# Kernel optimization log

Measured on AMD Instinct MI355X. Metric: run time of the kernel, lower is better.

The kernel has to match this reference:

```python
import jax, jax.numpy as jnp
import numpy as np

NUM_CLASSES = 512
WIDTH = 2  # triangular half-width in bins
MODE = 'triangular'
SIGMA = 1.0
B = 65536


def setup_inputs() -> dict:
    key = jax.random.key(0)
    k1, k2 = jax.random.split(key)
    logits = jax.random.normal(k1, (B, NUM_CLASSES), dtype=jnp.float32)
    targets = jax.random.randint(k2, (B,), 0, NUM_CLASSES, dtype=jnp.int64)
    return {"logits": logits, "targets": targets}


def _soft_targets(targets, C, dtype):
    # Vectorized replacement of the per-row Python loop.
    c = targets[:, None]                     # [B, 1]
    j = jnp.arange(C)[None, :]               # [1, C]
    d = jnp.abs(j - c)                       # [B, C] bin distance
    if MODE == 'triangular':
        w = jnp.where(d <= WIDTH, (WIDTH + 1 - d).astype(dtype), jnp.zeros((), dtype))
    elif MODE == 'log-triangular':
        w = jnp.where(d <= WIDTH, jnp.exp(-d.astype(dtype)), jnp.zeros((), dtype))
    else:  # gaussian
        w = jnp.where(d <= WIDTH,
                      jnp.exp(-0.5 * (d.astype(dtype) / SIGMA) ** 2),
                      jnp.zeros((), dtype))
    return w / jnp.sum(w, axis=1, keepdims=True)


def reference(logits, targets):
    Bsz, C = logits.shape
    st = _soft_targets(targets, C, logits.dtype)        # [B, C] normalized soft labels
    logp = jax.nn.log_softmax(logits, axis=1)            # [B, C]
    # KL(st || softmax(logits)) with 0*log0 = 0, matching F.kl_div(log_probs, st)
    safe_st = jnp.where(st > 0, st, jnp.ones((), logits.dtype))
    kl = jnp.where(st > 0, st * (jnp.log(safe_st) - logp), jnp.zeros((), logits.dtype))
    return jnp.sum(kl) / Bsz  # batchmean
```

## Files before the change

kernel.cpp:

```cpp
#include <hip/hip_runtime.h>

#define CDIM 512
#define BROWS 65536
#define NBLK 4096

typedef float floatx4 __attribute__((ext_vector_type(4)));

__device__ __forceinline__ float wpart(int j, int t, float x) {
    int d = j - t;
    int ad = d < 0 ? -d : d;
    return (ad <= 2) ? (float)(3 - ad) * x : 0.0f;
}

__global__ __launch_bounds__(256) void SoftTargetLoss_62646392979666_kernel(
        const float* __restrict__ logits,
        const int* __restrict__ targets,
        float* __restrict__ partials) {
    const int lane = threadIdx.x & 63;
    const int wid  = threadIdx.x >> 6;
    const int row0 = (blockIdx.x * 4 + wid) * 4;

    floatx4 a[4], b[4];
    int t[4];
    #pragma unroll
    for (int r = 0; r < 4; ++r) {
        const floatx4* rp = (const floatx4*)(logits + (size_t)(row0 + r) * CDIM);
        a[r] = __builtin_nontemporal_load(rp + lane);
        b[r] = __builtin_nontemporal_load(rp + lane + 64);
    }
    #pragma unroll
    for (int r = 0; r < 4; ++r) t[r] = targets[row0 + r];

    float acc = 0.0f;
    float s[4];
    #pragma unroll
    for (int r = 0; r < 4; ++r) {
        s[r] = __expf(a[r].x) + __expf(a[r].y) + __expf(a[r].z) + __expf(a[r].w)
             + __expf(b[r].x) + __expf(b[r].y) + __expf(b[r].z) + __expf(b[r].w);

        const int j0 = lane * 4, j1 = 256 + lane * 4;
        const int tt = t[r];
        float dp = wpart(j0,     tt, a[r].x) + wpart(j0 + 1, tt, a[r].y)
                 + wpart(j0 + 2, tt, a[r].z) + wpart(j0 + 3, tt, a[r].w)
                 + wpart(j1,     tt, b[r].x) + wpart(j1 + 1, tt, b[r].y)
                 + wpart(j1 + 2, tt, b[r].z) + wpart(j1 + 3, tt, b[r].w);

        float H, invW;
        if (tt >= 2 && tt <= CDIM - 3) { H = -1.52295508f; invW = 1.0f / 9.0f; }
        else if (tt == 0 || tt == CDIM - 1) { H = -1.01140427f; invW = 1.0f / 6.0f; }
        else { H = -1.32088835f; invW = 1.0f / 8.0f; }

        acc = fmaf(dp, -invW, acc);
        acc += H * (1.0f / 64.0f);
    }

    #pragma unroll
    for (int off = 32; off >= 1; off >>= 1) {
        #pragma unroll
        for (int r = 0; r < 4; ++r) s[r] += __shfl_xor(s[r], off, 64);
    }
    #pragma unroll
    for (int r = 0; r < 4; ++r) acc += __logf(s[r]) * (1.0f / 64.0f);

    #pragma unroll
    for (int off = 32; off >= 1; off >>= 1) acc += __shfl_xor(acc, off, 64);

    __shared__ float sred[4];
    if (lane == 0) sred[wid] = acc;
    __syncthreads();
    if (threadIdx.x == 0)
        partials[blockIdx.x] = sred[0] + sred[1] + sred[2] + sred[3];
}

__global__ __launch_bounds__(256) void stl_reduce(
        const float* __restrict__ partials, float* __restrict__ out) {
    float v = 0.0f;
    for (int i = threadIdx.x; i < NBLK; i += 256) v += partials[i];
    #pragma unroll
    for (int off = 32; off >= 1; off >>= 1) v += __shfl_xor(v, off, 64);
    __shared__ float sred[4];
    if ((threadIdx.x & 63) == 0) sred[threadIdx.x >> 6] = v;
    __syncthreads();
    if (threadIdx.x == 0)
        out[0] = (sred[0] + sred[1] + sred[2] + sred[3]) * (1.0f / (float)BROWS);
}

extern "C" void kernel_launch(void* const* d_in, const int* in_sizes, int n_in,
                              void* d_out, int out_size, void* d_ws, size_t ws_size,
                              hipStream_t stream) {
    const float* logits   = (const float*)d_in[0];
    const int*   targets  = (const int*)d_in[1];
    float*       out      = (float*)d_out;
    float*       partials = (float*)d_ws;

    SoftTargetLoss_62646392979666_kernel<<<NBLK, 256, 0, stream>>>(logits, targets, partials);
    stl_reduce<<<1, 256, 0, stream>>>(partials, out);
}
```

Before: 183.1 us.

## Process 16 rows per wave with double-buffered register prefetch

Each wave now handles 16 rows in four iterations instead of 4 rows. The loads for the next group of 4 rows are issued before computing the current group, using two register buffers, and the grid shrinks to 1024 blocks with a launch-bounds occupancy hint. This is meant to overlap memory latency with the exp and shuffle work and to cut block launch overhead and partials traffic, at the cost of higher register pressure and fewer waves for latency hiding. The final reduce loop is also unrolled over the smaller partials array.

Measured after the change: 217.2 us. 1.19x slower.

```diff
diff --git a/kernel.cpp b/kernel.cpp
--- a/kernel.cpp
+++ b/kernel.cpp
@@ -2,7 +2,8 @@
 
 #define CDIM 512
 #define BROWS 65536
-#define NBLK 4096
+#define NBLK 1024
+#define ITERS 4
 
 typedef float floatx4 __attribute__((ext_vector_type(4)));
 
@@ -12,55 +13,73 @@
     return (ad <= 2) ? (float)(3 - ad) * x : 0.0f;
 }
 
-__global__ __launch_bounds__(256) void SoftTargetLoss_62646392979666_kernel(
+__global__ __launch_bounds__(256, 4) void SoftTargetLoss_62646392979666_kernel(
         const float* __restrict__ logits,
         const int* __restrict__ targets,
         float* __restrict__ partials) {
     const int lane = threadIdx.x & 63;
     const int wid  = threadIdx.x >> 6;
-    const int row0 = (blockIdx.x * 4 + wid) * 4;
+    const int gw   = blockIdx.x * 4 + wid;
+    const size_t row0 = (size_t)gw * (ITERS * 4);
+    const floatx4* rp = (const floatx4*)logits + row0 * (CDIM / 4);
 
-    floatx4 a[4], b[4];
-    int t[4];
+    int t[ITERS * 4];
+    #pragma unroll
+    for (int r = 0; r < ITERS * 4; ++r) t[r] = targets[row0 + r];
+
+    floatx4 A[2][4], B[2][4];
     #pragma unroll
     for (int r = 0; r < 4; ++r) {
-        const floatx4* rp = (const floatx4*)(logits + (size_t)(row0 + r) * CDIM);
-        a[r] = __builtin_nontemporal_load(rp + lane);
-        b[r] = __builtin_nontemporal_load(rp + lane + 64);
+        A[0][r] = __builtin_nontemporal_load(rp + (size_t)r * (CDIM / 4) + lane);
+        B[0][r] = __builtin_nontemporal_load(rp + (size_t)r * (CDIM / 4) + 64 + lane);
     }
-    #pragma unroll
-    for (int r = 0; r < 4; ++r) t[r] = targets[row0 + r];
 
     float acc = 0.0f;
-    float s[4];
-    #pragma unroll
-    for (int r = 0; r < 4; ++r) {
-        s[r] = __expf(a[r].x) + __expf(a[r].y) + __expf(a[r].z) + __expf(a[r].w)
-             + __expf(b[r].x) + __expf(b[r].y) + __expf(b[r].z) + __expf(b[r].w);
-
-        const int j0 = lane * 4, j1 = 256 + lane * 4;
-        const int tt = t[r];
-        float dp = wpart(j0,     tt, a[r].x) + wpart(j0 + 1, tt, a[r].y)
-                 + wpart(j0 + 2, tt, a[r].z) + wpart(j0 + 3, tt, a[r].w)
-                 + wpart(j1,     tt, b[r].x) + wpart(j1 + 1, tt, b[r].y)
-                 + wpart(j1 + 2, tt, b[r].z) + wpart(j1 + 3, tt, b[r].w);
-
-        float H, invW;
-        if (tt >= 2 && tt <= CDIM - 3) { H = -1.52295508f; invW = 1.0f / 9.0f; }
-        else if (tt == 0 || tt == CDIM - 1) { H = -1.01140427f; invW = 1.0f / 6.0f; }
-        else { H = -1.32088835f; invW = 1.0f / 8.0f; }
-
-        acc = fmaf(dp, -invW, acc);
-        acc += H * (1.0f / 64.0f);
-    }
 
     #pragma unroll
-    for (int off = 32; off >= 1; off >>= 1) {
+    for (int it = 0; it < ITERS; ++it) {
+        const int cb = it & 1;
+        if (it + 1 < ITERS) {
+            const int nb = cb ^ 1;
+            #pragma unroll
+            for (int r = 0; r < 4; ++r) {
+                const size_t v = (size_t)(it + 1) * 4 * (CDIM / 4) + (size_t)r * (CDIM / 4);
+                A[nb][r] = __builtin_nontemporal_load(rp + v + lane);
+                B[nb][r] = __builtin_nontemporal_load(rp + v + 64 + lane);
+            }
+        }
+
+        float s[4];
         #pragma unroll
-        for (int r = 0; r < 4; ++r) s[r] += __shfl_xor(s[r], off, 64);
+        for (int r = 0; r < 4; ++r) {
+            const floatx4 a = A[cb][r], b = B[cb][r];
+            s[r] = __expf(a.x) + __expf(a.y) + __expf(a.z) + __expf(a.w)
+                 + __expf(b.x) + __expf(b.y) + __expf(b.z) + __expf(b.w);
+
+            const int j0 = lane * 4, j1 = 256 + lane * 4;
+            const int tt = t[it * 4 + r];
+            float dp = wpart(j0,     tt, a.x) + wpart(j0 + 1, tt, a.y)
+                     + wpart(j0 + 2, tt, a.z) + wpart(j0 + 3, tt, a.w)
+                     + wpart(j1,     tt, b.x) + wpart(j1 + 1, tt, b.y)
+                     + wpart(j1 + 2, tt, b.z) + wpart(j1 + 3, tt, b.w);
+
+            float H, invW;
+            if (tt >= 2 && tt <= CDIM - 3) { H = -1.52295508f; invW = 1.0f / 9.0f; }
+            else if (tt == 0 || tt == CDIM - 1) { H = -1.01140427f; invW = 1.0f / 6.0f; }
+            else { H = -1.32088835f; invW = 1.0f / 8.0f; }
+
+            acc = fmaf(dp, -invW, acc);
+            acc += H * (1.0f / 64.0f);
+        }
+
+        #pragma unroll
+        for (int off = 32; off >= 1; off >>= 1) {
+            #pragma unroll
+            for (int r = 0; r < 4; ++r) s[r] += __shfl_xor(s[r], off, 64);
+        }
+        #pragma unroll
+        for (int r = 0; r < 4; ++r) acc += __logf(s[r]) * (1.0f / 64.0f);
     }
-    #pragma unroll
-    for (int r = 0; r < 4; ++r) acc += __logf(s[r]) * (1.0f / 64.0f);
 
     #pragma unroll
     for (int off = 32; off >= 1; off >>= 1) acc += __shfl_xor(acc, off, 64);
@@ -75,7 +94,8 @@
 __global__ __launch_bounds__(256) void stl_reduce(
         const float* __restrict__ partials, float* __restrict__ out) {
     float v = 0.0f;
-    for (int i = threadIdx.x; i < NBLK; i += 256) v += partials[i];
+    #pragma unroll
+    for (int i = 0; i < NBLK / 256; ++i) v += partials[threadIdx.x + i * 256];
     #pragma unroll
     for (int off = 32; off >= 1; off >>= 1) v += __shfl_xor(v, off, 64);
     __shared__ float sred[4];
```

## Process one row per wavefront with 4x more blocks and vectorized final reduce

Applied to the files above, without the earlier changes.

Each wavefront now handles a single row instead of four, so the grid grows from 4096 to 16384 blocks. Fewer bytes are in flight per thread, but there are more waves to hide memory latency. The per-row loss combination moves after the reductions: the dot product is reduced across lanes alongside the exp-sum, and one lane computes H + log(s) - dp*invW. The final reduce kernel now reads partials as float4 vectors over the larger partial array.

New measurement: 179.5 us. No clear change (-1.9%).

```diff
diff --git a/kernel.cpp b/kernel.cpp
--- a/kernel.cpp
+++ b/kernel.cpp
@@ -2,7 +2,7 @@
 
 #define CDIM 512
 #define BROWS 65536
-#define NBLK 4096
+#define NBLK 16384
 
 typedef float floatx4 __attribute__((ext_vector_type(4)));
 
@@ -18,55 +18,35 @@
         float* __restrict__ partials) {
     const int lane = threadIdx.x & 63;
     const int wid  = threadIdx.x >> 6;
-    const int row0 = (blockIdx.x * 4 + wid) * 4;
+    const int row  = blockIdx.x * 4 + wid;
 
-    floatx4 a[4], b[4];
-    int t[4];
-    #pragma unroll
-    for (int r = 0; r < 4; ++r) {
-        const floatx4* rp = (const floatx4*)(logits + (size_t)(row0 + r) * CDIM);
-        a[r] = __builtin_nontemporal_load(rp + lane);
-        b[r] = __builtin_nontemporal_load(rp + lane + 64);
-    }
-    #pragma unroll
-    for (int r = 0; r < 4; ++r) t[r] = targets[row0 + r];
+    const floatx4* rp = (const floatx4*)(logits + (size_t)row * CDIM);
+    floatx4 a = __builtin_nontemporal_load(rp + lane);
+    floatx4 b = __builtin_nontemporal_load(rp + lane + 64);
+    const int tt = targets[row];
 
-    float acc = 0.0f;
-    float s[4];
-    #pragma unroll
-    for (int r = 0; r < 4; ++r) {
-        s[r] = __expf(a[r].x) + __expf(a[r].y) + __expf(a[r].z) + __expf(a[r].w)
-             + __expf(b[r].x) + __expf(b[r].y) + __expf(b[r].z) + __expf(b[r].w);
+    float s = __expf(a.x) + __expf(a.y) + __expf(a.z) + __expf(a.w)
+            + __expf(b.x) + __expf(b.y) + __expf(b.z) + __expf(b.w);
 
-        const int j0 = lane * 4, j1 = 256 + lane * 4;
-        const int tt = t[r];
-        float dp = wpart(j0,     tt, a[r].x) + wpart(j0 + 1, tt, a[r].y)
-                 + wpart(j0 + 2, tt, a[r].z) + wpart(j0 + 3, tt, a[r].w)
-                 + wpart(j1,     tt, b[r].x) + wpart(j1 + 1, tt, b[r].y)
-                 + wpart(j1 + 2, tt, b[r].z) + wpart(j1 + 3, tt, b[r].w);
-
-        float H, invW;
-        if (tt >= 2 && tt <= CDIM - 3) { H = -1.52295508f; invW = 1.0f / 9.0f; }
-        else if (tt == 0 || tt == CDIM - 1) { H = -1.01140427f; invW = 1.0f / 6.0f; }
-        else { H = -1.32088835f; invW = 1.0f / 8.0f; }
-
-        acc = fmaf(dp, -invW, acc);
-        acc += H * (1.0f / 64.0f);
-    }
+    const int j0 = lane * 4, j1 = 256 + lane * 4;
+    float dp = wpart(j0,     tt, a.x) + wpart(j0 + 1, tt, a.y)
+             + wpart(j0 + 2, tt, a.z) + wpart(j0 + 3, tt, a.w)
+             + wpart(j1,     tt, b.x) + wpart(j1 + 1, tt, b.y)
+             + wpart(j1 + 2, tt, b.z) + wpart(j1 + 3, tt, b.w);
 
     #pragma unroll
     for (int off = 32; off >= 1; off >>= 1) {
-        #pragma unroll
-        for (int r = 0; r < 4; ++r) s[r] += __shfl_xor(s[r], off, 64);
+        s  += __shfl_xor(s,  off, 64);
+        dp += __shfl_xor(dp, off, 64);
     }
-    #pragma unroll
-    for (int r = 0; r < 4; ++r) acc += __logf(s[r]) * (1.0f / 64.0f);
 
-    #pragma unroll
-    for (int off = 32; off >= 1; off >>= 1) acc += __shfl_xor(acc, off, 64);
+    float H, invW;
+    if (tt >= 2 && tt <= CDIM - 3) { H = -1.52295508f; invW = 1.0f / 9.0f; }
+    else if (tt == 0 || tt == CDIM - 1) { H = -1.01140427f; invW = 1.0f / 6.0f; }
+    else { H = -1.32088835f; invW = 1.0f / 8.0f; }
 
     __shared__ float sred[4];
-    if (lane == 0) sred[wid] = acc;
+    if (lane == 0) sred[wid] = H + __logf(s) - dp * invW;
     __syncthreads();
     if (threadIdx.x == 0)
         partials[blockIdx.x] = sred[0] + sred[1] + sred[2] + sred[3];
@@ -74,8 +54,11 @@
 
 __global__ __launch_bounds__(256) void stl_reduce(
         const float* __restrict__ partials, float* __restrict__ out) {
-    float v = 0.0f;
-    for (int i = threadIdx.x; i < NBLK; i += 256) v += partials[i];
+    const floatx4* p4 = (const floatx4*)partials;
+    floatx4 v4 = {0.f, 0.f, 0.f, 0.f};
+    #pragma unroll
+    for (int i = 0; i < NBLK / 4 / 256; ++i) v4 += p4[threadIdx.x + i * 256];
+    float v = v4.x + v4.y + v4.z + v4.w;
     #pragma unroll
     for (int off = 32; off >= 1; off >>= 1) v += __shfl_xor(v, off, 64);
     __shared__ float sred[4];
```
